# Performance work log

Measured on AMD Instinct MI355X. Metric: run time of the kernel, lower is better.

Reference implementation:

```python
import jax, jax.numpy as jnp
import numpy as np

B, S, D, H, K = 1, 4096, 1024, 16, 64


def setup_inputs() -> dict:
    key = jax.random.key(0)
    ks = jax.random.split(key, 5)
    x = jax.random.normal(ks[0], (B, S, D), dtype=jnp.float32)
    wq = jax.random.normal(ks[1], (D, H, K), dtype=jnp.float32) / np.sqrt(D)
    wk = jax.random.normal(ks[2], (D, H, K), dtype=jnp.float32) / np.sqrt(D)
    wv = jax.random.normal(ks[3], (D, H, K), dtype=jnp.float32) / np.sqrt(D)
    wo = jax.random.normal(ks[4], (H, K, D), dtype=jnp.float32) / np.sqrt(H * K)
    bq = jnp.zeros((H, K), dtype=jnp.float32)
    bk = jnp.zeros((H, K), dtype=jnp.float32)
    bv = jnp.zeros((H, K), dtype=jnp.float32)
    bo = jnp.zeros((D,), dtype=jnp.float32)
    return {"x": x, "wq": wq, "bq": bq, "wk": wk, "bk": bk,
            "wv": wv, "bv": bv, "wo": wo, "bo": bo, "is_causal": 1}


def reference(x, wq, bq, wk, bk, wv, bv, wo, bo, is_causal):
    # QKV projections: [B,S,D] x [D,H,K] -> [B,S,H,K]
    q = jnp.einsum("bsd,dhk->bshk", x, wq) + bq
    k = jnp.einsum("bsd,dhk->bshk", x, wk) + bk
    v = jnp.einsum("bsd,dhk->bshk", x, wv) + bv
    # scores: [B,H,Q,KV], scaled by 1/sqrt(head_dim)
    scores = jnp.einsum("bqhk,bvhk->bhqv", q, k) / jnp.sqrt(jnp.float32(K))
    if is_causal:
        qpos = jnp.arange(S)[:, None]  # query position
        kpos = jnp.arange(S)[None, :]  # key position
        mask = (qpos >= kpos).astype(scores.dtype)  # [Q,KV]
        scores = scores - 1e9 * (1.0 - mask)
    probs = jax.nn.softmax(scores, axis=-1)
    # weighted values: [B,S,H,K]
    vals = jnp.einsum("bhqv,bvhk->bqhk", probs, v)
    # output projection: [B,S,H,K] x [H,K,D] -> [B,S,D]
    out = jnp.einsum("bqhk,hkd->bqd", vals, wo) + bo
    return out
```

## Files before the change

### kernel.cpp

```cpp
#include <hip/hip_runtime.h>

typedef _Float16 f16;
typedef f16 f16x8 __attribute__((ext_vector_type(8)));
typedef f16 f16x4 __attribute__((ext_vector_type(4)));
typedef float f32x4 __attribute__((ext_vector_type(4)));
typedef float f32x16 __attribute__((ext_vector_type(16)));
typedef unsigned u32;

#define MFMA16(a, b, c) __builtin_amdgcn_mfma_f32_16x16x32_f16((a), (b), (c), 0, 0, 0)
#define MFMA32(a, b, c) __builtin_amdgcn_mfma_f32_32x32x16_f16((a), (b), (c), 0, 0, 0)

#define QSCL 0.18033688011f

#define WAITV(N) asm volatile("s_waitcnt vmcnt(" #N ")" ::: "memory")
#define BAR()                          \
  {                                    \
    __builtin_amdgcn_s_barrier();      \
    __builtin_amdgcn_sched_barrier(0); \
  }

__device__ __forceinline__ void gll16(const void* g, void* l) {
  __builtin_amdgcn_global_load_lds(
      (__attribute__((address_space(1))) unsigned int*)(void*)(g),
      (__attribute__((address_space(3))) unsigned int*)(l), 16, 0, 0);
}

__device__ __forceinline__ float ex2(float x) {
  float r;
  asm("v_exp_f32 %0, %1" : "=v"(r) : "v"(x));
  return r;
}

__device__ __forceinline__ void plswap(u32& a, u32& b) {
  asm("s_nop 1\n\tv_permlane32_swap_b32 %0, %1\n\ts_nop 1" : "+v"(a), "+v"(b));
}

__device__ __forceinline__ u32 pk16(float lo, float hi) {
  __fp16 h2[2];
  *(decltype(__builtin_amdgcn_cvt_pkrtz(0.f, 0.f))*)h2 =
      __builtin_amdgcn_cvt_pkrtz(lo, hi);
  return *(u32*)h2;
}

__global__ void k_prep(const float* __restrict__ x, f16* __restrict__ xb,
                       const float* __restrict__ wq, const float* __restrict__ wk,
                       const float* __restrict__ wv, const float* __restrict__ wo,
                       f16* __restrict__ wqkvT, f16* __restrict__ woT) {
  __shared__ float tile[64][65];
  const int bid = blockIdx.x;
  if (bid < 4096) {
    const int i = bid * 256 + threadIdx.x;
    float4 v = reinterpret_cast<const float4*>(x)[i];
    f16x4 o = {(f16)v.x, (f16)v.y, (f16)v.z, (f16)v.w};
    reinterpret_cast<f16x4*>(xb)[i] = o;
    return;
  }
  const int tb = bid - 4096;
  const int which = tb >> 8;
  const int bidx = tb & 255;
  const float* src = which == 0 ? wq : which == 1 ? wk : which == 2 ? wv : wo;
  f16* dst = which == 0 ? wqkvT
             : which == 1 ? wqkvT + (size_t)1024 * 1024
             : which == 2 ? wqkvT + (size_t)2048 * 1024
                          : woT;
  const int bc = bidx & 15, br = bidx >> 4;
  const int r0 = br << 6, c0 = bc << 6;
  const int tr = threadIdx.x >> 6, tc = threadIdx.x & 63;
#pragma unroll
  for (int p = 0; p < 16; ++p)
    tile[p * 4 + tr][tc] = src[(size_t)(r0 + p * 4 + tr) * 1024 + c0 + tc];
  __syncthreads();
#pragma unroll
  for (int p = 0; p < 16; ++p)
    dst[(size_t)(c0 + p * 4 + tr) * 1024 + r0 + tc] = (f16)tile[tc][p * 4 + tr];
}

template <int MODE, int NFR, int PAIR>
__global__ __launch_bounds__(256, 3) void k_gemm(
    const f16* __restrict__ A, const f16* __restrict__ Bt, int nbm, int Kd,
    const float* __restrict__ bias0, const float* __restrict__ bias1,
    const float* __restrict__ bias2,
    f16* __restrict__ Qo, f16* __restrict__ Ko, f16* __restrict__ Vo,
    float* __restrict__ Fo) {
  constexpr int TSZ = 8192 + NFR * 2048;
  constexpr int NBUF = PAIR ? 4 : 3;
  __shared__ __align__(16) char smem[NBUF * TSZ];
  const int tid = threadIdx.x;
  const int wid = tid >> 6, lane = tid & 63;
  const int r = lane & 15, t = lane >> 4;
  const int bm = blockIdx.x % nbm, bn = blockIdx.x / nbm;
  const int m0 = bm << 7, n0 = bn * (NFR * 32);
  const int wr = wid >> 1, wc = wid & 1;

  const f32x4 vz = {0.f, 0.f, 0.f, 0.f};
  f32x4 acc[4][NFR];
#pragma unroll
  for (int m = 0; m < 4; ++m)
#pragma unroll
    for (int n = 0; n < NFR; ++n) acc[m][n] = vz;

  const int srow = tid >> 2;
  const int scb = (((tid & 3) ^ ((tid >> 3) & 3)) << 4);
  const size_t ldb = (size_t)Kd * 2;
  const char* Ab = (const char*)A + (size_t)m0 * ldb + scb;
  const char* Bb = (const char*)Bt + (size_t)n0 * ldb + scb;

  auto issue = [&](int kt, int buf) {
    const size_t kb = (size_t)kt << 6;
    char* base = smem + buf * TSZ;
    gll16(Ab + (size_t)srow * ldb + kb, base + wid * 1024);
    gll16(Ab + (size_t)(srow + 64) * ldb + kb, base + 4096 + wid * 1024);
    gll16(Bb + (size_t)srow * ldb + kb, base + 8192 + wid * 1024);
    if (NFR == 4)
      gll16(Bb + (size_t)(srow + 64) * ldb + kb, base + 8192 + 4096 + wid * 1024);
  };

  const int swz = ((r >> 1) & 3) << 4;

  auto comp = [&](int buf) {
    const char* base = smem + buf * TSZ;
    f16x8 af[4], bg[NFR];
#pragma unroll
    for (int m = 0; m < 4; ++m)
      af[m] = *(const f16x8*)(base + ((wr * 64 + m * 16 + r) * 64 +
                                      ((t * 16) ^ swz)));
#pragma unroll
    for (int n = 0; n < NFR; ++n)
      bg[n] = *(const f16x8*)(base + 8192 +
                              ((wc * (NFR * 16) + n * 16 + r) * 64 +
                               ((t * 16) ^ swz)));
    __builtin_amdgcn_s_setprio(1);
#pragma unroll
    for (int m = 0; m < 4; ++m)
#pragma unroll
      for (int n = 0; n < NFR; ++n) acc[m][n] = MFMA16(af[m], bg[n], acc[m][n]);
    __builtin_amdgcn_s_setprio(0);
  };

  const int nk = Kd >> 5;
  if (PAIR) {
    issue(0, 0);
    issue(1, 1);
    const int nsup = nk >> 1;
    for (int T = 0; T < nsup; ++T) {
      WAITV(0);
      BAR();
      if (T + 1 < nsup) {
        issue(2 * T + 2, (2 * T + 2) & 3);
        issue(2 * T + 3, (2 * T + 3) & 3);
      }
      comp((2 * T) & 3);
      comp((2 * T + 1) & 3);
    }
  } else {
    issue(0, 0);
    issue(1, 1);
    int b = 0, bi = 2;
    for (int kt = 0; kt < nk; ++kt) {
      if (kt + 1 < nk) {
        if (NFR == 4) {
          WAITV(4);
        } else {
          WAITV(3);
        }
      } else {
        WAITV(0);
      }
      BAR();
      if (kt + 2 < nk) issue(kt + 2, bi);
      comp(b);
      b = (b == 2) ? 0 : b + 1;
      bi = (bi == 2) ? 0 : bi + 1;
    }
  }

#pragma unroll
  for (int m = 0; m < 4; ++m) {
    const int row0 = m0 + wr * 64 + m * 16 + t * 4;
#pragma unroll
    for (int n = 0; n < NFR; ++n) {
      const int gc = n0 + wc * (NFR * 16) + n * 16 + r;
      if (MODE == 0) {
        const float b2 = gc < 1024 ? bias0[gc]
                                   : (gc < 2048 ? bias1[gc - 1024] : bias2[gc - 2048]);
        float v[4];
#pragma unroll
        for (int i = 0; i < 4; ++i) v[i] = acc[m][n][i] + b2;
        if (gc < 1024) {
#pragma unroll
          for (int i = 0; i < 4; ++i)
            Qo[(size_t)(row0 + i) * 1024 + gc] = (f16)(v[i] * QSCL);
        } else if (gc < 2048) {
#pragma unroll
          for (int i = 0; i < 4; ++i)
            Ko[(size_t)(row0 + i) * 1024 + (gc - 1024)] = (f16)v[i];
        } else {
          f16x4 pk = {(f16)v[0], (f16)v[1], (f16)v[2], (f16)v[3]};
          *(f16x4*)(Vo + (size_t)(gc - 2048) * 4096 + row0) = pk;
        }
      } else {
        const float b2 = bias0[gc];
#pragma unroll
        for (int i = 0; i < 4; ++i)
          Fo[(size_t)(row0 + i) * 1024 + gc] = acc[m][n][i] + b2;
      }
    }
  }
}

__global__ __launch_bounds__(512, 4) void k_fattn(
    const f16* __restrict__ Q, const f16* __restrict__ Kb,
    const f16* __restrict__ Vt, f16* __restrict__ vals,
    const int* __restrict__ causp) {
  __shared__ uint4 ldsv[4128];
  char* lds = (char*)ldsv;
  const int tid = threadIdx.x;
  const int W = tid >> 6, lane = tid & 63;
  const int l31 = lane & 31, hi = lane >> 5;
  const int wq = W >> 1, wkv = W & 1;
  const int h = blockIdx.x & 15;
  const int idx = blockIdx.x >> 4;
  const int qt = idx < 16 ? 31 - idx : idx - 16;
  const int cz = *causp;
  const int Tmax = cz ? qt : 31;
  const int dw = wq - wkv;
  const int jmax_w = cz ? (2 * qt + (dw >= 2 ? 1 : 0) - (dw < 0 ? 1 : 0)) : 63;
  const bool maskd = cz && ((dw & 1) == 0);

  const size_t qrow = (size_t)((qt << 7) + (wq << 5) + l31) * 1024 + h * 64;
  f16x8 qf[4];
#pragma unroll
  for (int s = 0; s < 4; ++s) qf[s] = *(const f16x8*)(Q + qrow + 16 * s + 8 * hi);

  f32x16 o0, o1, zv;
#pragma unroll
  for (int e = 0; e < 16; ++e) { o0[e] = 0.f; o1[e] = 0.f; zv[e] = 0.f; }
  float Ls = 0.f;

  const int srw = lane >> 3, sch = lane & 7;
  const int ssw = (sch ^ srw) << 3;
  const char* kcur =
      (const char*)(Kb + (size_t)(8 * W + srw) * 1024 + h * 64 + ssw);
  const char* vcur =
      (const char*)(Vt + (size_t)(h * 64 + 8 * W + srw) * 4096 + ssw);

  auto issue = [&](int buf) {
    char* base = lds + buf * 16384 + W * 1024;
    gll16(kcur, base);
    gll16(vcur, base + 8192);
    kcur += (size_t)64 * 2048;
    vcur += 128;
  };

  const int krow = (wkv << 5) + l31, ksw = krow & 7;
  const int vsw = l31 & 7;

  auto qk = [&](const char* Kbase) -> f32x16 {
    f16x8 af[4];
#pragma unroll
    for (int s = 0; s < 4; ++s)
      af[s] = *(const f16x8*)(Kbase + krow * 128 + (((2 * s + hi) ^ ksw) << 4));
    __builtin_amdgcn_s_setprio(1);
    f32x16 sc = MFMA32(af[0], qf[0], zv);
#pragma unroll
    for (int s = 1; s < 4; ++s) sc = MFMA32(af[s], qf[s], sc);
    __builtin_amdgcn_s_setprio(0);
    return sc;
  };

  auto fin = [&](int j, const char* Kbase, f32x16& sc) {
    const char* Vbase = Kbase + 8192;
    if (maskd && j == jmax_w) {
#pragma unroll
      for (int e = 0; e < 16; ++e) {
        const int kvr = (e & 3) + 8 * (e >> 2) + 4 * hi;
        if (kvr > l31) sc[e] = -1e9f;
      }
    }
    float p[16];
#pragma unroll
    for (int e = 0; e < 16; ++e) p[e] = ex2(sc[e]);
    {
      float s0 = (p[0] + p[1]) + (p[2] + p[3]);
      float s1 = (p[4] + p[5]) + (p[6] + p[7]);
      float s2 = (p[8] + p[9]) + (p[10] + p[11]);
      float s3 = (p[12] + p[13]) + (p[14] + p[15]);
      float s = (s0 + s1) + (s2 + s3);
      union { float f; u32 u; } ua, ub;
      ua.f = s; ub.f = s;
      plswap(ua.u, ub.u);
      Ls += ua.f + ub.f;
    }
#pragma unroll
    for (int ks = 0; ks < 2; ++ks) {
      u32 c0 = pk16(p[8 * ks + 0], p[8 * ks + 1]);
      u32 c1 = pk16(p[8 * ks + 2], p[8 * ks + 3]);
      u32 c2 = pk16(p[8 * ks + 4], p[8 * ks + 5]);
      u32 c3 = pk16(p[8 * ks + 6], p[8 * ks + 7]);
      plswap(c0, c2);
      plswap(c1, c3);
      union { u32 w[4]; f16x8 v; } pa;
      pa.w[0] = c0; pa.w[1] = c1; pa.w[2] = c2; pa.w[3] = c3;
      const int cl = 4 * wkv + 2 * ks + hi;
      const f16x8 vf0 = *(const f16x8*)(Vbase + l31 * 128 + ((cl ^ vsw) << 4));
      const f16x8 vf1 =
          *(const f16x8*)(Vbase + (32 + l31) * 128 + ((cl ^ vsw) << 4));
      __builtin_amdgcn_s_setprio(1);
      o0 = MFMA32(pa.v, vf0, o0);
      o1 = MFMA32(pa.v, vf1, o1);
      __builtin_amdgcn_s_setprio(0);
    }
  };

  issue(0);
  issue(1);

  for (int T = 0; T <= Tmax; ++T) {
    BAR();
    if (T < Tmax) {
      const int nb = 2 * ((T + 1) & 1);
      issue(nb);
      issue(nb + 1);
      WAITV(4);
    } else {
      WAITV(0);
    }
    const int cb = 2 * (T & 1);
    const char* bA = lds + cb * 16384;
    const char* bB = lds + (cb + 1) * 16384;
    const int jA = 2 * T, jB = 2 * T + 1;
    if (jB <= jmax_w) {
      f32x16 scA = qk(bA);
      f32x16 scB = qk(bB);
      fin(jA, bA, scA);
      fin(jB, bB, scB);
    } else if (jA <= jmax_w) {
      f32x16 scA = qk(bA);
      fin(jA, bA, scA);
    }
  }
  __syncthreads();

  float* obuf = (float*)lds;
  float* lsbuf = (float*)(lds + 32768);
  if (hi == 0) lsbuf[wq * 64 + wkv * 32 + l31] = Ls;
  if (wkv == 1) {
    float* base = obuf + wq * 2048;
#pragma unroll
    for (int dblk = 0; dblk < 2; ++dblk)
#pragma unroll
      for (int rg = 0; rg < 4; ++rg) {
        const f32x16& o = dblk ? o1 : o0;
        f32x4 t = {o[rg * 4 + 0], o[rg * 4 + 1], o[rg * 4 + 2], o[rg * 4 + 3]};
        *(f32x4*)(base + ((dblk * 4 + rg) * 64 + lane) * 4) = t;
      }
  }
  __syncthreads();
  if (wkv == 0) {
    float* base = obuf + wq * 2048;
#pragma unroll
    for (int dblk = 0; dblk < 2; ++dblk)
#pragma unroll
      for (int rg = 0; rg < 4; ++rg) {
        f32x4 t = *(f32x4*)(base + ((dblk * 4 + rg) * 64 + lane) * 4);
        f32x16& o = dblk ? o1 : o0;
#pragma unroll
        for (int i = 0; i < 4; ++i) o[rg * 4 + i] += t[i];
      }
    float inv[16];
#pragma unroll
    for (int e = 0; e < 16; ++e) {
      const int q = (e & 3) + 8 * (e >> 2) + 4 * hi;
      inv[e] = 1.0f / (lsbuf[wq * 64 + q] + lsbuf[wq * 64 + 32 + q]);
    }
    const int row0 = (qt << 7) + (wq << 5);
#pragma unroll
    for (int dblk = 0; dblk < 2; ++dblk) {
      const f32x16& o = dblk ? o1 : o0;
      const int col = h * 64 + 32 * dblk + l31;
#pragma unroll
      for (int e = 0; e < 16; ++e) {
        const int rr = row0 + (e & 3) + 8 * (e >> 2) + 4 * hi;
        vals[(size_t)rr * 1024 + col] = (f16)(o[e] * inv[e]);
      }
    }
  }
}

extern "C" void kernel_launch(void* const* d_in, const int* in_sizes, int n_in,
                              void* d_out, int out_size, void* d_ws, size_t ws_size,
                              hipStream_t stream) {
  const float* x = (const float*)d_in[0];
  const float* wq = (const float*)d_in[1];
  const float* bq = (const float*)d_in[2];
  const float* wk = (const float*)d_in[3];
  const float* bk = (const float*)d_in[4];
  const float* wv = (const float*)d_in[5];
  const float* bv = (const float*)d_in[6];
  const float* wo = (const float*)d_in[7];
  const float* bo = (const float*)d_in[8];
  const int* caus = (const int*)d_in[9];
  float* out = (float*)d_out;

  f16* xb = (f16*)d_ws;
  f16* wqkvT = xb + (size_t)4096 * 1024;
  f16* woT = wqkvT + (size_t)3072 * 1024;
  f16* Qb = woT + (size_t)1024 * 1024;
  f16* Kbuf = Qb + (size_t)4096 * 1024;
  f16* Vt = Kbuf + (size_t)4096 * 1024;
  f16* vals = Vt + (size_t)4096 * 1024;

  k_prep<<<5120, 256, 0, stream>>>(x, xb, wq, wk, wv, wo, wqkvT, woT);
  k_gemm<0, 4, 0><<<32 * 24, 256, 0, stream>>>(xb, wqkvT, 32, 1024, bq, bk, bv,
                                               Qb, Kbuf, Vt, nullptr);
  k_fattn<<<512, 512, 0, stream>>>(Qb, Kbuf, Vt, vals, caus);
  k_gemm<1, 2, 1><<<32 * 16, 256, 0, stream>>>(vals, woT, 32, 1024, bo, nullptr,
                                               nullptr, nullptr, nullptr,
                                               nullptr, out);
}
```

Measured before the change: 117.3 us.

## Split long causal query tiles across two KV chunks with a merge kernel

The attention kernel now splits the KV range of the 16 heaviest query tiles per head into two chunks, each handled by its own block, using constant lookup tables that order the work. Grid size goes from 512 to 768 blocks. Split blocks write unnormalized fp16 partial outputs and row sums into reused workspace, and a new k_fix kernel adds and normalizes them. This targets load imbalance and tail effects in causal attention, at the cost of an extra launch, extra partial-result traffic, and fp16 rounding of the unnormalized partial outputs.

```diff
diff --git a/kernel.cpp b/kernel.cpp
--- a/kernel.cpp
+++ b/kernel.cpp
@@ -208,10 +208,20 @@
   }
 }
 
+__constant__ unsigned char g_qt[48] = {
+    15, 30, 31, 31, 14, 28, 29, 29, 30, 13, 26, 27, 27, 28, 12, 24,
+    25, 25, 26, 11, 22, 23, 23, 24, 10, 20, 21, 21, 22, 9,  18, 19,
+    19, 20, 8,  16, 17, 17, 18, 7,  16, 6,  5,  4,  3,  2,  1,  0};
+__constant__ unsigned char g_ch[48] = {
+    2, 0, 0, 1, 2, 0, 0, 1, 1, 2, 0, 0, 1, 1, 2, 0,
+    0, 1, 1, 2, 0, 0, 1, 1, 2, 0, 0, 1, 1, 2, 0, 0,
+    1, 1, 2, 0, 0, 1, 1, 2, 1, 2, 2, 2, 2, 2, 2, 2};
+
 __global__ __launch_bounds__(512, 4) void k_fattn(
     const f16* __restrict__ Q, const f16* __restrict__ Kb,
     const f16* __restrict__ Vt, f16* __restrict__ vals,
-    const int* __restrict__ causp) {
+    const int* __restrict__ causp, f16* __restrict__ part_o,
+    float* __restrict__ part_ls) {
   __shared__ uint4 ldsv[4128];
   char* lds = (char*)ldsv;
   const int tid = threadIdx.x;
@@ -219,10 +229,22 @@
   const int l31 = lane & 31, hi = lane >> 5;
   const int wq = W >> 1, wkv = W & 1;
   const int h = blockIdx.x & 15;
-  const int idx = blockIdx.x >> 4;
-  const int qt = idx < 16 ? 31 - idx : idx - 16;
+  const int it = blockIdx.x >> 4;
+  const int qt = g_qt[it];
+  const int ch = g_ch[it];
   const int cz = *causp;
-  const int Tmax = cz ? qt : 31;
+  int Tstart, tlen;
+  if (ch == 2) {
+    Tstart = 0;
+    tlen = cz ? qt + 1 : 32;
+  } else if (ch == 0) {
+    Tstart = 0;
+    tlen = cz ? (qt + 2) >> 1 : 16;
+  } else {
+    Tstart = cz ? (qt + 2) >> 1 : 16;
+    tlen = cz ? (qt + 1) >> 1 : 16;
+  }
+  const int Tend = Tstart + tlen - 1;
   const int dw = wq - wkv;
   const int jmax_w = cz ? (2 * qt + (dw >= 2 ? 1 : 0) - (dw < 0 ? 1 : 0)) : 63;
   const bool maskd = cz && ((dw & 1) == 0);
@@ -240,9 +262,11 @@
   const int srw = lane >> 3, sch = lane & 7;
   const int ssw = (sch ^ srw) << 3;
   const char* kcur =
-      (const char*)(Kb + (size_t)(8 * W + srw) * 1024 + h * 64 + ssw);
+      (const char*)(Kb + (size_t)(8 * W + srw) * 1024 + h * 64 + ssw) +
+      (size_t)Tstart * 262144;
   const char* vcur =
-      (const char*)(Vt + (size_t)(h * 64 + 8 * W + srw) * 4096 + ssw);
+      (const char*)(Vt + (size_t)(h * 64 + 8 * W + srw) * 4096 + ssw) +
+      (size_t)Tstart * 256;
 
   auto issue = [&](int buf) {
     char* base = lds + buf * 16384 + W * 1024;
@@ -312,12 +336,15 @@
     }
   };
 
-  issue(0);
-  issue(1);
-
-  for (int T = 0; T <= Tmax; ++T) {
+  {
+    const int pb = 2 * (Tstart & 1);
+    issue(pb);
+    issue(pb + 1);
+  }
+
+  for (int T = Tstart; T <= Tend; ++T) {
     BAR();
-    if (T < Tmax) {
+    if (T < Tend) {
       const int nb = 2 * ((T + 1) & 1);
       issue(nb);
       issue(nb + 1);
@@ -356,7 +383,10 @@
       }
   }
   __syncthreads();
-  if (wkv == 0) {
+
+  float lst[16];
+  const bool writer = (wkv == 0);
+  if (writer) {
     float* base = obuf + wq * 2048;
 #pragma unroll
     for (int dblk = 0; dblk < 2; ++dblk)
@@ -367,23 +397,79 @@
 #pragma unroll
         for (int i = 0; i < 4; ++i) o[rg * 4 + i] += t[i];
       }
-    float inv[16];
 #pragma unroll
     for (int e = 0; e < 16; ++e) {
       const int q = (e & 3) + 8 * (e >> 2) + 4 * hi;
-      inv[e] = 1.0f / (lsbuf[wq * 64 + q] + lsbuf[wq * 64 + 32 + q]);
-    }
-    const int row0 = (qt << 7) + (wq << 5);
+      lst[e] = lsbuf[wq * 64 + q] + lsbuf[wq * 64 + 32 + q];
+    }
+  }
+
+  if (ch == 2) {
+    if (writer) {
+      const int row0 = (qt << 7) + (wq << 5);
+#pragma unroll
+      for (int dblk = 0; dblk < 2; ++dblk) {
+        const f32x16& o = dblk ? o1 : o0;
+        const int col = h * 64 + 32 * dblk + l31;
+#pragma unroll
+        for (int e = 0; e < 16; ++e) {
+          const int rr = row0 + (e & 3) + 8 * (e >> 2) + 4 * hi;
+          vals[(size_t)rr * 1024 + col] = (f16)(o[e] / lst[e]);
+        }
+      }
+    }
+    return;
+  }
+
+  if (writer) {
+    const int tix = h * 16 + (qt - 16);
+    const int slot = (tix << 1) | ch;
+    f16* po = part_o + (size_t)slot * 8192;
+    float* pl = part_ls + slot * 128;
 #pragma unroll
     for (int dblk = 0; dblk < 2; ++dblk) {
       const f32x16& o = dblk ? o1 : o0;
-      const int col = h * 64 + 32 * dblk + l31;
+      const int col = 32 * dblk + l31;
 #pragma unroll
       for (int e = 0; e < 16; ++e) {
-        const int rr = row0 + (e & 3) + 8 * (e >> 2) + 4 * hi;
-        vals[(size_t)rr * 1024 + col] = (f16)(o[e] * inv[e]);
-      }
-    }
+        const int rr = 32 * wq + (e & 3) + 8 * (e >> 2) + 4 * hi;
+        po[rr * 64 + col] = (f16)o[e];
+      }
+    }
+    if (l31 == 0) {
+#pragma unroll
+      for (int e = 0; e < 16; ++e) {
+        const int q = (e & 3) + 8 * (e >> 2) + 4 * hi;
+        pl[32 * wq + q] = lst[e];
+      }
+    }
+  }
+}
+
+__global__ __launch_bounds__(256) void k_fix(const f16* __restrict__ part_o,
+                                             const float* __restrict__ part_ls,
+                                             f16* __restrict__ vals) {
+  const int tix = blockIdx.x;
+  const int h = tix >> 4, qt = 16 + (tix & 15);
+  const int t = threadIdx.x;
+  const int row = t >> 1, c0 = (t & 1) * 32;
+  const f16* po0 = part_o + (((size_t)tix << 1) | 0) * 8192;
+  const f16* po1 = part_o + (((size_t)tix << 1) | 1) * 8192;
+  const float ls = part_ls[((tix << 1) | 0) * 128 + row] +
+                   part_ls[((tix << 1) | 1) * 128 + row];
+  const float inv = 1.0f / ls;
+  const f16* a = po0 + row * 64 + c0;
+  const f16* b = po1 + row * 64 + c0;
+  f16* d = vals + (size_t)((qt << 7) + row) * 1024 + h * 64 + c0;
+#pragma unroll
+  for (int i = 0; i < 4; ++i) {
+    f16x8 va = *(const f16x8*)(a + 8 * i);
+    f16x8 vb = *(const f16x8*)(b + 8 * i);
+    f16x8 vo;
+#pragma unroll
+    for (int j = 0; j < 8; ++j)
+      vo[j] = (f16)(((float)va[j] + (float)vb[j]) * inv);
+    *(f16x8*)(d + 8 * i) = vo;
   }
 }
 
@@ -410,10 +496,14 @@
   f16* Vt = Kbuf + (size_t)4096 * 1024;
   f16* vals = Vt + (size_t)4096 * 1024;
 
+  f16* part_o = xb;
+  float* part_ls = (float*)wqkvT;
+
   k_prep<<<5120, 256, 0, stream>>>(x, xb, wq, wk, wv, wo, wqkvT, woT);
   k_gemm<0, 4, 0><<<32 * 24, 256, 0, stream>>>(xb, wqkvT, 32, 1024, bq, bk, bv,
                                                Qb, Kbuf, Vt, nullptr);
-  k_fattn<<<512, 512, 0, stream>>>(Qb, Kbuf, Vt, vals, caus);
+  k_fattn<<<768, 512, 0, stream>>>(Qb, Kbuf, Vt, vals, caus, part_o, part_ls);
+  k_fix<<<256, 256, 0, stream>>>(part_o, part_ls, vals);
   k_gemm<1, 2, 1><<<32 * 16, 256, 0, stream>>>(vals, woT, 32, 1024, bo, nullptr,
                                                nullptr, nullptr, nullptr,
                                                nullptr, out);
```

New measurement: 120.4 us. 1.03x slower.
